# Optimization experiments

Hardware: AMD Instinct MI355X
Metric: run time of the kernel (lower is better)

The kernel has to match this reference:

```python
import jax, jax.numpy as jnp
import numpy as np

D = 768          # TGLU_hidden_dim == input_hidden_dim
E = 8            # num_experts
TOP_K = 2        # top_experts
N_ENT = 32       # num_entity
B = 16           # batch (mentions)
L = 128          # max_seq_len
EPS = 1e-5


def setup_inputs() -> dict:
    key = jax.random.key(0)
    ks = jax.random.split(key, 16)
    s = 0.02
    return {
        "entity_text_cls": jax.random.normal(ks[0], (N_ENT, D), jnp.float32),
        "entity_text_tokens": jax.random.normal(ks[1], (N_ENT, L, D), jnp.float32),
        "mention_text_cls": jax.random.normal(ks[2], (B, D), jnp.float32),
        "mention_text_tokens": jax.random.normal(ks[3], (B, L, D), jnp.float32),
        # SwitchMoE params: gate + per-expert Linear(dim -> output_dim)
        "gate_w": jax.random.normal(ks[4], (D, E), jnp.float32) * s,
        "gate_b": jnp.zeros((E,), jnp.float32),
        "exp_w": jax.random.normal(ks[5], (E, D, D), jnp.float32) * s,
        "exp_b": jnp.zeros((E, D), jnp.float32),
        # attention projections
        "wq": jax.random.normal(ks[6], (D, D), jnp.float32) * s,
        "bq": jnp.zeros((D,), jnp.float32),
        "wk": jax.random.normal(ks[7], (D, D), jnp.float32) * s,
        "bk": jnp.zeros((D,), jnp.float32),
        "wv": jax.random.normal(ks[8], (D, D), jnp.float32) * s,
        "bv": jnp.zeros((D,), jnp.float32),
        # LayerNorm params
        "ln_w": jnp.ones((D,), jnp.float32),
        "ln_b": jnp.zeros((D,), jnp.float32),
    }


def _switch_moe(x, gate_w, gate_b, exp_w, exp_b):
    # x: [n, s, D] -> [n, s, D]; top-k router, renormalized combine.
    logits = jnp.einsum("nsd,de->nse", x, gate_w) + gate_b
    probs = jax.nn.softmax(logits, axis=-1)
    vals, idx = jax.lax.top_k(probs, TOP_K)              # [n,s,k]
    vals = vals / jnp.sum(vals, axis=-1, keepdims=True)
    # combine weights over all experts (zero for unselected) -> dense mask form
    w = jnp.sum(jax.nn.one_hot(idx, E, dtype=x.dtype) * vals[..., None], axis=-2)  # [n,s,E]
    eo = jnp.einsum("nsd,edo->nseo", x, exp_w) + exp_b   # [n,s,E,D]
    return jnp.einsum("nse,nseo->nso", w, eo)


def _layernorm(x, w, b):
    mu = jnp.mean(x, axis=-1, keepdims=True)
    var = jnp.mean(jnp.square(x - mu), axis=-1, keepdims=True)
    return (x - mu) * jax.lax.rsqrt(var + EPS) * w + b


def reference(entity_text_cls, entity_text_tokens, mention_text_cls, mention_text_tokens,
              gate_w, gate_b, exp_w, exp_b, wq, bq, wk, bk, wv, bv, ln_w, ln_b):
    # prepend CLS, route through shared MoE
    ent = jnp.concatenate([entity_text_cls[:, None, :], entity_text_tokens], axis=1)   # [N,L+1,D]
    ent_moe = _switch_moe(ent, gate_w, gate_b, exp_w, exp_b)
    ent_cls_moe = ent_moe[:, 0, :]          # [N,D]
    ent_tok = ent_moe[:, 1:, :]             # [N,L,D]

    men = jnp.concatenate([mention_text_cls[:, None, :], mention_text_tokens], axis=1)  # [B,L+1,D]
    men_moe = _switch_moe(men, gate_w, gate_b, exp_w, exp_b)
    men_tok = men_moe[:, 1:, :]             # [B,L,D]

    q = jnp.einsum("nld,do->nlo", ent_tok, wq) + bq    # [N,L,D]
    k = jnp.einsum("bmd,do->bmo", men_tok, wk) + bk    # [B,L,D]
    v = jnp.einsum("bmd,do->bmo", men_tok, wv) + bv    # [B,L,D]

    # all-pairs entity x mention cross attention: [N,B,L,L]
    scores = jnp.einsum("nld,bmd->nblm", q, k) / jnp.sqrt(jnp.asarray(D, q.dtype))
    probs = jax.nn.softmax(scores, axis=-1)
    context = jnp.einsum("nblm,bmd->nbld", probs, v)   # [N,B,L,D]
    context = jnp.mean(context, axis=-2)               # [N,B,D]
    context = _layernorm(context, ln_w, ln_b)

    g2l = jnp.sum(ent_cls_moe[:, None, :] * context, axis=-1)   # [N,B]
    g2l = g2l.T                                                  # [B,N]
    g2g = mention_text_cls @ entity_text_cls.T                   # [B,N]
    return (g2l + g2g) / 2
```

## Files before the change

kernel.cpp:

```cpp
#include <hip/hip_runtime.h>
#include <math.h>

#define D 768
#define NE 8
#define NTOK 6192
#define MEN_TOK0 4128

typedef __attribute__((ext_vector_type(8))) short short8;
typedef __attribute__((ext_vector_type(4))) short short4b;
typedef __attribute__((ext_vector_type(4))) float floatx4;

__device__ __forceinline__ short f2bf(float f) {
  union { float f; unsigned u; } x; x.f = f;
  unsigned r = x.u + 0x7fffu + ((x.u >> 16) & 1u);
  return (short)(r >> 16);
}
__device__ __forceinline__ float bf2f(short s) {
  union { unsigned u; float f; } x; x.u = ((unsigned)(unsigned short)s) << 16;
  return x.f;
}

__device__ __forceinline__ void gload16(const short* g, short8* lds_base) {
  __builtin_amdgcn_global_load_lds(
      (const __attribute__((address_space(1))) unsigned int*)g,
      (__attribute__((address_space(3))) unsigned int*)lds_base,
      16, 0, 0);
}

#define PIPE_BAR(NSTR)                                            \
  do {                                                            \
    asm volatile("s_waitcnt vmcnt(" NSTR ")" ::: "memory");       \
    __builtin_amdgcn_sched_barrier(0);                            \
    __builtin_amdgcn_s_barrier();                                 \
    __builtin_amdgcn_sched_barrier(0);                            \
  } while (0)

__device__ __forceinline__ const float* token_row(int t,
    const float* __restrict__ ecls, const float* __restrict__ etok,
    const float* __restrict__ mcls, const float* __restrict__ mtok) {
  if (t < MEN_TOK0) {
    int n = t / 129, s = t - n * 129;
    return (s == 0) ? (ecls + n * D) : (etok + (size_t)(n * 128 + s - 1) * D);
  } else {
    int tm = t - MEN_TOK0;
    int b = tm / 129, s = tm - b * 129;
    return (s == 0) ? (mcls + b * D) : (mtok + (size_t)(b * 128 + s - 1) * D);
  }
}

__global__ __launch_bounds__(256) void prep_kernel(
    const float* __restrict__ ecls, const float* __restrict__ etok,
    const float* __restrict__ mcls, const float* __restrict__ mtok,
    const float* __restrict__ gate_w, const float* __restrict__ gate_b,
    const float* __restrict__ exp_w, const float* __restrict__ wq,
    const float* __restrict__ wk, const float* __restrict__ wv,
    int* __restrict__ te1, int* __restrict__ te2,
    float* __restrict__ tw1, float* __restrict__ tw2,
    short* __restrict__ Xb, short* __restrict__ expwT, short* __restrict__ wT) {
  __shared__ float tbuf[64][65];
  int bid = blockIdx.x;
  int tid = threadIdx.x;
  if (bid < 1548) {
    int t = bid * 4 + (tid >> 6);
    int lane = tid & 63;
    const float* xr = token_row(t, ecls, etok, mcls, mtok);
    float acc[NE];
#pragma unroll
    for (int e = 0; e < NE; ++e) acc[e] = 0.f;
#pragma unroll
    for (int it = 0; it < 3; ++it) {
      int d0 = lane * 4 + it * 256;
      floatx4 x = *(const floatx4*)(xr + d0);
      short4b xb;
#pragma unroll
      for (int q = 0; q < 4; ++q) {
        xb[q] = f2bf(x[q]);
        float xv = x[q];
#pragma unroll
        for (int e = 0; e < NE; ++e) acc[e] += xv * gate_w[(d0 + q) * NE + e];
      }
      *(short4b*)(Xb + (size_t)t * D + d0) = xb;
    }
#pragma unroll
    for (int e = 0; e < NE; ++e) {
#pragma unroll
      for (int off = 32; off > 0; off >>= 1) acc[e] += __shfl_down(acc[e], off);
    }
    if (lane == 0) {
      float lg[NE];
#pragma unroll
      for (int e = 0; e < NE; ++e) lg[e] = acc[e] + gate_b[e];
      int e1 = 0;
#pragma unroll
      for (int e = 1; e < NE; ++e) if (lg[e] > lg[e1]) e1 = e;
      int e2 = (e1 == 0) ? 1 : 0;
#pragma unroll
      for (int e = 0; e < NE; ++e) {
        if (e != e1 && lg[e] > lg[e2]) e2 = e;
      }
      float w1 = 1.f / (1.f + __expf(lg[e2] - lg[e1]));
      te1[t] = e1; te2[t] = e2;
      tw1[t] = w1; tw2[t] = 1.f - w1;
    }
  } else {
    int zz = bid - 1548;
    int z = zz / 144, rem = zz % 144;
    int k0 = (rem / 12) * 64, o0 = (rem % 12) * 64;
    const float* src; short* dst;
    if (z < 8) { src = exp_w + (size_t)z * D * D; dst = expwT + (size_t)z * D * D; }
    else { src = (z == 8) ? wq : (z == 9) ? wk : wv; dst = wT + (size_t)(z - 8) * D * D; }
    int tx = tid & 63, ty = tid >> 6;
#pragma unroll
    for (int i = 0; i < 16; ++i) {
      int k = i * 4 + ty;
      tbuf[k][tx] = src[(size_t)(k0 + k) * D + o0 + tx];
    }
    __syncthreads();
#pragma unroll
    for (int i = 0; i < 16; ++i) {
      int o = i * 4 + ty;
      dst[(size_t)(o0 + o) * D + k0 + tx] = f2bf(tbuf[tx][o]);
    }
  }
}

__global__ __launch_bounds__(1024) void route_kernel(
    const int* __restrict__ te1, const int* __restrict__ te2,
    int* __restrict__ lst_tok, int* __restrict__ slot1, int* __restrict__ slot2,
    int* __restrict__ cnt, int* __restrict__ basee) {
  __shared__ int hist[NE];
  __shared__ int base_s[NE];
  int tid = threadIdx.x;
  if (tid < NE) hist[tid] = 0;
  __syncthreads();
  for (int t = tid; t < NTOK; t += 1024) {
    atomicAdd(&hist[te1[t]], 1);
    atomicAdd(&hist[te2[t]], 1);
  }
  __syncthreads();
  if (tid == 0) {
    int acc = 0;
    for (int e = 0; e < NE; ++e) {
      base_s[e] = acc;
      cnt[e] = hist[e];
      basee[e] = acc;
      acc += hist[e];
    }
  }
  __syncthreads();
  if (tid < NE) hist[tid] = 0;
  __syncthreads();
  for (int t = tid; t < NTOK; t += 1024) {
    int e1 = te1[t], e2 = te2[t];
    int r1 = atomicAdd(&hist[e1], 1);
    int r2 = atomicAdd(&hist[e2], 1);
    int s1 = base_s[e1] + r1;
    int s2 = base_s[e2] + r2;
    slot1[t] = s1; slot2[t] = s2;
    lst_tok[s1] = t; lst_tok[s2] = t;
  }
}

__global__ __launch_bounds__(512, 4) void moe_kernel(
    const short* __restrict__ Xb, const short* __restrict__ expwT,
    const int* __restrict__ cnt, const int* __restrict__ basee,
    const int* __restrict__ lst_tok, short* __restrict__ EO) {
  int id = blockIdx.x;
  int e = id & 7;
  int r = id >> 3;
  int ob = r % 6;
  int tb = r / 6;
  int count = cnt[e];
  int t0 = tb * 128;
  if (t0 >= count) return;
  int o0 = ob * 128;
  int gb = basee[e];

  __shared__ short8 As[1536];
  __shared__ short8 Bs[1536];
  __shared__ int stok[128];

  int tid = threadIdx.x;
  int l = tid & 63, w = tid >> 6;
  int wr = w >> 1, wc = w & 1;

  if (tid < 128) {
    int p = t0 + tid;
    stok[tid] = lst_tok[gb + (p < count ? p : 0)];
  }
  __syncthreads();

  const short* Bg = expwT + (size_t)e * D * D;
  int srow = tid >> 2, scc = tid & 3;
  int csrc = (scc ^ ((srow >> 1) & 3)) * 8;
  const short* srcA = Xb + (size_t)stok[srow] * D + csrc;
  const short* srcB = Bg + (size_t)(o0 + srow) * D + csrc;

  floatx4 acc[2][4];
#pragma unroll
  for (int ai = 0; ai < 2; ++ai)
#pragma unroll
    for (int bj = 0; bj < 4; ++bj) acc[ai][bj] = (floatx4){0.f, 0.f, 0.f, 0.f};

  gload16(srcA, &As[w << 6]);
  gload16(srcB, &Bs[w << 6]);
  gload16(srcA + 32, &As[512 + (w << 6)]);
  gload16(srcB + 32, &Bs[512 + (w << 6)]);

  for (int it = 0; it < 24; ++it) {
    if (it < 23) PIPE_BAR("2"); else PIPE_BAR("0");
    int cur = (it % 3) << 9;
    if (it < 22) {
      int nb = ((it + 2) % 3) << 9;
      int k0n = (it + 2) * 32;
      gload16(srcA + k0n, &As[nb + (w << 6)]);
      gload16(srcB + k0n, &Bs[nb + (w << 6)]);
    }
    int kc = l >> 4;
    short8 a[2], bb[4];
#pragma unroll
    for (int ai = 0; ai < 2; ++ai) {
      int ar = wr * 32 + ai * 16 + (l & 15);
      a[ai] = As[cur + (ar << 2) + (kc ^ ((ar >> 1) & 3))];
    }
#pragma unroll
    for (int bj = 0; bj < 4; ++bj) {
      int br = wc * 64 + bj * 16 + (l & 15);
      bb[bj] = Bs[cur + (br << 2) + (kc ^ ((br >> 1) & 3))];
    }
    __builtin_amdgcn_s_setprio(1);
#pragma unroll
    for (int ai = 0; ai < 2; ++ai)
#pragma unroll
      for (int bj = 0; bj < 4; ++bj)
        acc[ai][bj] = __builtin_amdgcn_mfma_f32_16x16x32_bf16(a[ai], bb[bj], acc[ai][bj], 0, 0, 0);
    __builtin_amdgcn_s_setprio(0);
  }

#pragma unroll
  for (int ai = 0; ai < 2; ++ai) {
#pragma unroll
    for (int rr = 0; rr < 4; ++rr) {
      int rowl = wr * 32 + ai * 16 + ((l >> 4) << 2) + rr;
      int p = t0 + rowl;
      if (p < count) {
        size_t off = (size_t)(gb + p) * D;
#pragma unroll
        for (int bj = 0; bj < 4; ++bj) {
          int col = o0 + wc * 64 + bj * 16 + (l & 15);
          EO[off + col] = f2bf(acc[ai][bj][rr]);
        }
      }
    }
  }
}

__global__ __launch_bounds__(256) void combine_kernel(
    const short* __restrict__ EO,
    const int* __restrict__ te1, const int* __restrict__ te2,
    const float* __restrict__ tw1, const float* __restrict__ tw2,
    const int* __restrict__ slot1, const int* __restrict__ slot2,
    const float* __restrict__ exp_b, short* __restrict__ MOEb) {
  int idx = blockIdx.x * 256 + threadIdx.x;
  int t = idx / 96, cg = idx - t * 96;
  int c0 = cg * 8;
  int e1 = te1[t], e2 = te2[t];
  float w1 = tw1[t], w2 = tw2[t];
  short8 a = *(const short8*)(EO + (size_t)slot1[t] * D + c0);
  short8 b = *(const short8*)(EO + (size_t)slot2[t] * D + c0);
  const float* b1 = exp_b + e1 * D + c0;
  const float* b2 = exp_b + e2 * D + c0;
  short8 o;
#pragma unroll
  for (int j = 0; j < 8; ++j)
    o[j] = f2bf(w1 * (bf2f(a[j]) + b1[j]) + w2 * (bf2f(b[j]) + b2[j]));
  *(short8*)(MOEb + (size_t)t * D + c0) = o;
}

__global__ __launch_bounds__(512, 4) void qkv_kernel(
    const short* __restrict__ MOEb, const short* __restrict__ wT,
    const float* __restrict__ bq, const float* __restrict__ bk,
    const float* __restrict__ bv,
    short* __restrict__ Qb, short* __restrict__ Kb, short* __restrict__ Vb) {
  int id = blockIdx.x;
  int z, r;
  if (id < 192)      { z = 0; r = id; }
  else if (id < 288) { z = 1; r = id - 192; }
  else               { z = 2; r = id - 288; }
  int tb = r / 6, ob = r % 6;
  int o0 = ob * 128;
  int base = (z == 0) ? 0 : MEN_TOK0;
  const short* W = wT + (size_t)z * D * D;
  const float* bias = (z == 0) ? bq : (z == 1) ? bk : bv;
  const short* Ag = MOEb + (size_t)(base + tb * 129 + 1) * D;

  __shared__ short8 As[1536];
  __shared__ short8 Bs[1536];

  int tid = threadIdx.x;
  int l = tid & 63, w = tid >> 6;
  int wr = w >> 1, wc = w & 1;

  int srow = tid >> 2, scc = tid & 3;
  int csrc = (scc ^ ((srow >> 1) & 3)) * 8;
  const short* srcA = Ag + (size_t)srow * D + csrc;
  const short* srcB = W + (size_t)(o0 + srow) * D + csrc;

  floatx4 acc[2][4];
#pragma unroll
  for (int ai = 0; ai < 2; ++ai)
#pragma unroll
    for (int bj = 0; bj < 4; ++bj) acc[ai][bj] = (floatx4){0.f, 0.f, 0.f, 0.f};

  gload16(srcA, &As[w << 6]);
  gload16(srcB, &Bs[w << 6]);
  gload16(srcA + 32, &As[512 + (w << 6)]);
  gload16(srcB + 32, &Bs[512 + (w << 6)]);

  for (int it = 0; it < 24; ++it) {
    if (it < 23) PIPE_BAR("2"); else PIPE_BAR("0");
    int cur = (it % 3) << 9;
    if (it < 22) {
      int nb = ((it + 2) % 3) << 9;
      int k0n = (it + 2) * 32;
      gload16(srcA + k0n, &As[nb + (w << 6)]);
      gload16(srcB + k0n, &Bs[nb + (w << 6)]);
    }
    int kc = l >> 4;
    short8 a[2], bb[4];
#pragma unroll
    for (int ai = 0; ai < 2; ++ai) {
      int ar = wr * 32 + ai * 16 + (l & 15);
      a[ai] = As[cur + (ar << 2) + (kc ^ ((ar >> 1) & 3))];
    }
#pragma unroll
    for (int bj = 0; bj < 4; ++bj) {
      int br = wc * 64 + bj * 16 + (l & 15);
      bb[bj] = Bs[cur + (br << 2) + (kc ^ ((br >> 1) & 3))];
    }
    __builtin_amdgcn_s_setprio(1);
#pragma unroll
    for (int ai = 0; ai < 2; ++ai)
#pragma unroll
      for (int bj = 0; bj < 4; ++bj)
        acc[ai][bj] = __builtin_amdgcn_mfma_f32_16x16x32_bf16(a[ai], bb[bj], acc[ai][bj], 0, 0, 0);
    __builtin_amdgcn_s_setprio(0);
  }

#pragma unroll
  for (int ai = 0; ai < 2; ++ai) {
#pragma unroll
    for (int rr = 0; rr < 4; ++rr) {
      int rowl = wr * 32 + ai * 16 + ((l >> 4) << 2) + rr;
      size_t rglob = (size_t)tb * 128 + rowl;
#pragma unroll
      for (int bj = 0; bj < 4; ++bj) {
        int col = o0 + wc * 64 + bj * 16 + (l & 15);
        float v = acc[ai][bj][rr] + bias[col];
        if (z == 0)      Qb[rglob * D + col] = f2bf(v);
        else if (z == 1) Kb[rglob * D + col] = f2bf(v);
        else             Vb[rglob * D + col] = f2bf(v);
      }
    }
  }
}

__device__ __forceinline__ float blockSum512(float v, volatile float* red, int tid) {
#pragma unroll
  for (int off = 32; off > 0; off >>= 1) v += __shfl_down(v, off);
  __syncthreads();
  if ((tid & 63) == 0) red[tid >> 6] = v;
  __syncthreads();
  float s = 0.f;
#pragma unroll
  for (int i = 0; i < 8; ++i) s += red[i];
  return s;
}

__global__ __launch_bounds__(512, 4) void attn_kernel(
    const short* __restrict__ Qb, const short* __restrict__ Kb,
    const short* __restrict__ Vb, const short* __restrict__ MOEb,
    const float* __restrict__ ecls, const float* __restrict__ mcls,
    const float* __restrict__ ln_w, const float* __restrict__ ln_b,
    float* __restrict__ out) {
  int id = blockIdx.x;
  int n = id & 31, b = id >> 5;
  __shared__ short8 Qs[1536];
  __shared__ short8 Ks[1536];
  __shared__ float pb[128];
  __shared__ float red[8];
  float* smm = (float*)Qs;
  float* sss = (float*)Qs + 256;
  int tid = threadIdx.x;
  int l = tid & 63, w = tid >> 6;
  int wr = w >> 1, wc = w & 1;
  if (tid < 128) pb[tid] = 0.f;
  __syncthreads();

  floatx4 acc[2][4];
#pragma unroll
  for (int ai = 0; ai < 2; ++ai)
#pragma unroll
    for (int bj = 0; bj < 4; ++bj) acc[ai][bj] = (floatx4){0.f, 0.f, 0.f, 0.f};

  const short* qg = Qb + (size_t)n * 128 * D;
  const short* kg = Kb + (size_t)b * 128 * D;

  int srow = tid >> 2, scc = tid & 3;
  int csrc = (scc ^ ((srow >> 1) & 3)) * 8;
  const short* srcQ = qg + (size_t)srow * D + csrc;
  const short* srcK = kg + (size_t)srow * D + csrc;

  gload16(srcQ, &Qs[w << 6]);
  gload16(srcK, &Ks[w << 6]);
  gload16(srcQ + 32, &Qs[512 + (w << 6)]);
  gload16(srcK + 32, &Ks[512 + (w << 6)]);

  for (int it = 0; it < 24; ++it) {
    if (it < 23) PIPE_BAR("2"); else PIPE_BAR("0");
    int cur = (it % 3) << 9;
    if (it < 22) {
      int nb = ((it + 2) % 3) << 9;
      int k0n = (it + 2) * 32;
      gload16(srcQ + k0n, &Qs[nb + (w << 6)]);
      gload16(srcK + k0n, &Ks[nb + (w << 6)]);
    }
    int kc = l >> 4;
    short8 a[2], bb[4];
#pragma unroll
    for (int ai = 0; ai < 2; ++ai) {
      int ar = wr * 32 + ai * 16 + (l & 15);
      a[ai] = Qs[cur + (ar << 2) + (kc ^ ((ar >> 1) & 3))];
    }
#pragma unroll
    for (int bj = 0; bj < 4; ++bj) {
      int br = wc * 64 + bj * 16 + (l & 15);
      bb[bj] = Ks[cur + (br << 2) + (kc ^ ((br >> 1) & 3))];
    }
    __builtin_amdgcn_s_setprio(1);
#pragma unroll
    for (int ai = 0; ai < 2; ++ai)
#pragma unroll
      for (int bj = 0; bj < 4; ++bj)
        acc[ai][bj] = __builtin_amdgcn_mfma_f32_16x16x32_bf16(a[ai], bb[bj], acc[ai][bj], 0, 0, 0);
    __builtin_amdgcn_s_setprio(0);
  }

  const float scale = 0.03608439182435161f;
  float mloc[2][4], sloc[2][4];
#pragma unroll
  for (int ai = 0; ai < 2; ++ai) {
#pragma unroll
    for (int r = 0; r < 4; ++r) {
      float mx = -3.0e38f;
#pragma unroll
      for (int bj = 0; bj < 4; ++bj) mx = fmaxf(mx, acc[ai][bj][r]);
      mx = fmaxf(mx, __shfl_xor(mx, 1));
      mx = fmaxf(mx, __shfl_xor(mx, 2));
      mx = fmaxf(mx, __shfl_xor(mx, 4));
      mx = fmaxf(mx, __shfl_xor(mx, 8));
      float sm = 0.f;
#pragma unroll
      for (int bj = 0; bj < 4; ++bj) {
        float pv = __expf((acc[ai][bj][r] - mx) * scale);
        acc[ai][bj][r] = pv;
        sm += pv;
      }
      sm += __shfl_xor(sm, 1);
      sm += __shfl_xor(sm, 2);
      sm += __shfl_xor(sm, 4);
      sm += __shfl_xor(sm, 8);
      mloc[ai][r] = mx;
      sloc[ai][r] = sm;
    }
  }
  __syncthreads();
  if ((l & 15) == 0) {
#pragma unroll
    for (int ai = 0; ai < 2; ++ai)
#pragma unroll
      for (int r = 0; r < 4; ++r) {
        int row = wr * 32 + ai * 16 + ((l >> 4) << 2) + r;
        smm[row * 2 + wc] = mloc[ai][r];
        sss[row * 2 + wc] = sloc[ai][r];
      }
  }
  __syncthreads();

  float colsum[4];
#pragma unroll
  for (int bj = 0; bj < 4; ++bj) colsum[bj] = 0.f;
#pragma unroll
  for (int ai = 0; ai < 2; ++ai) {
#pragma unroll
    for (int r = 0; r < 4; ++r) {
      int row = wr * 32 + ai * 16 + ((l >> 4) << 2) + r;
      float m0 = smm[row * 2], m1 = smm[row * 2 + 1];
      float s0 = sss[row * 2], s1 = sss[row * 2 + 1];
      float M = fmaxf(m0, m1);
      float Z = s0 * __expf((m0 - M) * scale) + s1 * __expf((m1 - M) * scale);
      float fac = __expf((mloc[ai][r] - M) * scale) / Z;
#pragma unroll
      for (int bj = 0; bj < 4; ++bj) colsum[bj] += acc[ai][bj][r] * fac;
    }
  }
#pragma unroll
  for (int bj = 0; bj < 4; ++bj) {
    colsum[bj] += __shfl_xor(colsum[bj], 16);
    colsum[bj] += __shfl_xor(colsum[bj], 32);
  }
  if (l < 16) {
#pragma unroll
    for (int bj = 0; bj < 4; ++bj)
      atomicAdd(&pb[wc * 64 + bj * 16 + l], colsum[bj]);
  }
  __syncthreads();

  float ctx[4] = {0.f, 0.f, 0.f, 0.f};
  bool act = tid < 192;
  int d0 = tid << 2;
  if (act) {
    const short* vb = Vb + (size_t)b * 128 * D + d0;
    for (int m = 0; m < 128; ++m) {
      float p = pb[m];
      short4b v = *(const short4b*)(vb + (size_t)m * D);
#pragma unroll
      for (int j = 0; j < 4; ++j) ctx[j] += p * bf2f(v[j]);
    }
#pragma unroll
    for (int j = 0; j < 4; ++j) ctx[j] *= (1.f / 128.f);
  }

  float mu = blockSum512(ctx[0] + ctx[1] + ctx[2] + ctx[3], red, tid) * (1.f / 768.f);
  float c[4];
#pragma unroll
  for (int j = 0; j < 4; ++j) c[j] = ctx[j] - mu;
  float vs = act ? (c[0]*c[0] + c[1]*c[1] + c[2]*c[2] + c[3]*c[3]) : 0.f;
  float var = blockSum512(vs, red, tid) * (1.f / 768.f);
  float rstd = rsqrtf(var + 1e-5f);

  float g2l_p = 0.f, g2g_p = 0.f;
  if (act) {
    floatx4 lw = *(const floatx4*)(ln_w + d0);
    floatx4 lb = *(const floatx4*)(ln_b + d0);
    short4b em = *(const short4b*)(MOEb + (size_t)(n * 129) * D + d0);
    floatx4 mc = *(const floatx4*)(mcls + (size_t)b * D + d0);
    floatx4 ec = *(const floatx4*)(ecls + (size_t)n * D + d0);
#pragma unroll
    for (int j = 0; j < 4; ++j) {
      float cl = c[j] * rstd * lw[j] + lb[j];
      g2l_p += bf2f(em[j]) * cl;
      g2g_p += mc[j] * ec[j];
    }
  }
  float g2l = blockSum512(g2l_p, red, tid);
  float g2g = blockSum512(g2g_p, red, tid);
  if (tid == 0) out[b * 32 + n] = 0.5f * (g2l + g2g);
}

extern "C" void kernel_launch(void* const* d_in, const int* in_sizes, int n_in,
                              void* d_out, int out_size, void* d_ws, size_t ws_size,
                              hipStream_t stream) {
  const float* ecls   = (const float*)d_in[0];
  const float* etok   = (const float*)d_in[1];
  const float* mcls   = (const float*)d_in[2];
  const float* mtok   = (const float*)d_in[3];
  const float* gate_w = (const float*)d_in[4];
  const float* gate_b = (const float*)d_in[5];
  const float* exp_w  = (const float*)d_in[6];
  const float* exp_b  = (const float*)d_in[7];
  const float* wq     = (const float*)d_in[8];
  const float* bq     = (const float*)d_in[9];
  const float* wk     = (const float*)d_in[10];
  const float* bk     = (const float*)d_in[11];
  const float* wv     = (const float*)d_in[12];
  const float* bv     = (const float*)d_in[13];
  const float* ln_w   = (const float*)d_in[14];
  const float* ln_b   = (const float*)d_in[15];
  float* outp = (float*)d_out;

  char* ws = (char*)d_ws;
  short* Qb    = (short*)(ws + 0);
  short* Kb    = (short*)(ws + 6291456);
  short* Vb    = (short*)(ws + 9437184);
  short* Xb    = (short*)(ws + 12582912);
  short* EO    = (short*)(ws + 22093824);
  short* MOEb  = (short*)(ws + 41115648);
  short* expwT = (short*)(ws + 50626560);
  short* wT    = (short*)(ws + 60063744);
  int*   te1   = (int*)  (ws + 63602688);
  int*   te2   = (int*)  (ws + 63627456);
  float* tw1   = (float*)(ws + 63652224);
  float* tw2   = (float*)(ws + 63676992);
  int*   slot1 = (int*)  (ws + 63701760);
  int*   slot2 = (int*)  (ws + 63726528);
  int*   lst_tok = (int*)(ws + 63751296);
  int*   cnt   = (int*)  (ws + 63800832);
  int*   basee = (int*)  (ws + 63800864);

  prep_kernel<<<1548 + 1584, 256, 0, stream>>>(ecls, etok, mcls, mtok, gate_w, gate_b,
                                               exp_w, wq, wk, wv,
                                               te1, te2, tw1, tw2, Xb, expwT, wT);
  route_kernel<<<1, 1024, 0, stream>>>(te1, te2, lst_tok, slot1, slot2, cnt, basee);
  moe_kernel<<<49 * 6 * 8, 512, 0, stream>>>(Xb, expwT, cnt, basee, lst_tok, EO);
  combine_kernel<<<2322, 256, 0, stream>>>(EO, te1, te2, tw1, tw2, slot1, slot2,
                                           exp_b, MOEb);
  qkv_kernel<<<384, 512, 0, stream>>>(MOEb, wT, bq, bk, bv, Qb, Kb, Vb);
  attn_kernel<<<512, 512, 0, stream>>>(Qb, Kb, Vb, MOEb, ecls, mcls, ln_w, ln_b, outp);
}
```

Baseline: 121.6 us.

## Fuse MoE combine into expert GEMM epilogue and QKV operand load

Removes the separate combine kernel. The MoE GEMM epilogue now applies the expert bias and routing weight and writes to one of two per-slot buffers (R1/R2) indexed by token. The QKV GEMM loads both buffers, sums them in registers and stores the result to LDS, replacing the async global-to-LDS A loads with a two-stage double buffer synchronised by __syncthreads. The route kernel uses per-wave histograms and packs the slot bit into the list entry. This saves one launch and a full read/write pass over the combined activations, at the cost of a less pipelined QKV A-path and an extra bf16 rounding before the sum.

```diff
diff --git a/kernel.cpp b/kernel.cpp
--- a/kernel.cpp
+++ b/kernel.cpp
@@ -126,45 +126,50 @@
 
 __global__ __launch_bounds__(1024) void route_kernel(
     const int* __restrict__ te1, const int* __restrict__ te2,
-    int* __restrict__ lst_tok, int* __restrict__ slot1, int* __restrict__ slot2,
-    int* __restrict__ cnt, int* __restrict__ basee) {
-  __shared__ int hist[NE];
-  __shared__ int base_s[NE];
+    int* __restrict__ lst, int* __restrict__ cnt, int* __restrict__ basee) {
+  __shared__ int wh[16][8];
+  __shared__ int wbase[16][8];
+  __shared__ int ctr[16][8];
+  __shared__ int gbase[8];
+  __shared__ int etot[8];
   int tid = threadIdx.x;
-  if (tid < NE) hist[tid] = 0;
+  int w = tid >> 6;
+  if (tid < 128) { ((int*)wh)[tid] = 0; ((int*)ctr)[tid] = 0; }
   __syncthreads();
   for (int t = tid; t < NTOK; t += 1024) {
-    atomicAdd(&hist[te1[t]], 1);
-    atomicAdd(&hist[te2[t]], 1);
+    atomicAdd(&wh[w][te1[t]], 1);
+    atomicAdd(&wh[w][te2[t]], 1);
+  }
+  __syncthreads();
+  if (tid < NE) {
+    int e = tid, acc = 0;
+    for (int ww = 0; ww < 16; ++ww) { wbase[ww][e] = acc; acc += wh[ww][e]; }
+    etot[e] = acc;
+    cnt[e] = acc;
   }
   __syncthreads();
   if (tid == 0) {
     int acc = 0;
-    for (int e = 0; e < NE; ++e) {
-      base_s[e] = acc;
-      cnt[e] = hist[e];
-      basee[e] = acc;
-      acc += hist[e];
-    }
-  }
-  __syncthreads();
-  if (tid < NE) hist[tid] = 0;
+    for (int e = 0; e < NE; ++e) { gbase[e] = acc; basee[e] = acc; acc += etot[e]; }
+  }
   __syncthreads();
   for (int t = tid; t < NTOK; t += 1024) {
-    int e1 = te1[t], e2 = te2[t];
-    int r1 = atomicAdd(&hist[e1], 1);
-    int r2 = atomicAdd(&hist[e2], 1);
-    int s1 = base_s[e1] + r1;
-    int s2 = base_s[e2] + r2;
-    slot1[t] = s1; slot2[t] = s2;
-    lst_tok[s1] = t; lst_tok[s2] = t;
+    int e1 = te1[t];
+    int r1 = atomicAdd(&ctr[w][e1], 1);
+    lst[gbase[e1] + wbase[w][e1] + r1] = (t << 1);
+    int e2 = te2[t];
+    int r2 = atomicAdd(&ctr[w][e2], 1);
+    lst[gbase[e2] + wbase[w][e2] + r2] = (t << 1) | 1;
   }
 }
 
 __global__ __launch_bounds__(512, 4) void moe_kernel(
     const short* __restrict__ Xb, const short* __restrict__ expwT,
     const int* __restrict__ cnt, const int* __restrict__ basee,
-    const int* __restrict__ lst_tok, short* __restrict__ EO) {
+    const int* __restrict__ lst,
+    const float* __restrict__ tw1, const float* __restrict__ tw2,
+    const float* __restrict__ exp_b,
+    short* __restrict__ R1, short* __restrict__ R2) {
   int id = blockIdx.x;
   int e = id & 7;
   int r = id >> 3;
@@ -186,14 +191,14 @@
 
   if (tid < 128) {
     int p = t0 + tid;
-    stok[tid] = lst_tok[gb + (p < count ? p : 0)];
+    stok[tid] = lst[gb + (p < count ? p : 0)];
   }
   __syncthreads();
 
   const short* Bg = expwT + (size_t)e * D * D;
   int srow = tid >> 2, scc = tid & 3;
   int csrc = (scc ^ ((srow >> 1) & 3)) * 8;
-  const short* srcA = Xb + (size_t)stok[srow] * D + csrc;
+  const short* srcA = Xb + (size_t)(stok[srow] >> 1) * D + csrc;
   const short* srcB = Bg + (size_t)(o0 + srow) * D + csrc;
 
   floatx4 acc[2][4];
@@ -237,6 +242,7 @@
     __builtin_amdgcn_s_setprio(0);
   }
 
+  const float* be = exp_b + e * D;
 #pragma unroll
   for (int ai = 0; ai < 2; ++ai) {
 #pragma unroll
@@ -244,41 +250,24 @@
       int rowl = wr * 32 + ai * 16 + ((l >> 4) << 2) + rr;
       int p = t0 + rowl;
       if (p < count) {
-        size_t off = (size_t)(gb + p) * D;
+        int ent = stok[rowl];
+        int tok = ent >> 1;
+        float wt = (ent & 1) ? tw2[tok] : tw1[tok];
+        short* OUT = (ent & 1) ? R2 : R1;
+        size_t off = (size_t)tok * D;
 #pragma unroll
         for (int bj = 0; bj < 4; ++bj) {
           int col = o0 + wc * 64 + bj * 16 + (l & 15);
-          EO[off + col] = f2bf(acc[ai][bj][rr]);
+          OUT[off + col] = f2bf(wt * (acc[ai][bj][rr] + be[col]));
         }
       }
     }
   }
 }
 
-__global__ __launch_bounds__(256) void combine_kernel(
-    const short* __restrict__ EO,
-    const int* __restrict__ te1, const int* __restrict__ te2,
-    const float* __restrict__ tw1, const float* __restrict__ tw2,
-    const int* __restrict__ slot1, const int* __restrict__ slot2,
-    const float* __restrict__ exp_b, short* __restrict__ MOEb) {
-  int idx = blockIdx.x * 256 + threadIdx.x;
-  int t = idx / 96, cg = idx - t * 96;
-  int c0 = cg * 8;
-  int e1 = te1[t], e2 = te2[t];
-  float w1 = tw1[t], w2 = tw2[t];
-  short8 a = *(const short8*)(EO + (size_t)slot1[t] * D + c0);
-  short8 b = *(const short8*)(EO + (size_t)slot2[t] * D + c0);
-  const float* b1 = exp_b + e1 * D + c0;
-  const float* b2 = exp_b + e2 * D + c0;
-  short8 o;
-#pragma unroll
-  for (int j = 0; j < 8; ++j)
-    o[j] = f2bf(w1 * (bf2f(a[j]) + b1[j]) + w2 * (bf2f(b[j]) + b2[j]));
-  *(short8*)(MOEb + (size_t)t * D + c0) = o;
-}
-
 __global__ __launch_bounds__(512, 4) void qkv_kernel(
-    const short* __restrict__ MOEb, const short* __restrict__ wT,
+    const short* __restrict__ R1, const short* __restrict__ R2,
+    const short* __restrict__ wT,
     const float* __restrict__ bq, const float* __restrict__ bk,
     const float* __restrict__ bv,
     short* __restrict__ Qb, short* __restrict__ Kb, short* __restrict__ Vb) {
@@ -292,10 +281,10 @@
   int base = (z == 0) ? 0 : MEN_TOK0;
   const short* W = wT + (size_t)z * D * D;
   const float* bias = (z == 0) ? bq : (z == 1) ? bk : bv;
-  const short* Ag = MOEb + (size_t)(base + tb * 129 + 1) * D;
-
-  __shared__ short8 As[1536];
-  __shared__ short8 Bs[1536];
+  int tok0 = base + tb * 129 + 1;
+
+  __shared__ short8 As[1024];
+  __shared__ short8 Bs[1024];
 
   int tid = threadIdx.x;
   int l = tid & 63, w = tid >> 6;
@@ -303,7 +292,8 @@
 
   int srow = tid >> 2, scc = tid & 3;
   int csrc = (scc ^ ((srow >> 1) & 3)) * 8;
-  const short* srcA = Ag + (size_t)srow * D + csrc;
+  const short* pR1 = R1 + (size_t)(tok0 + srow) * D + csrc;
+  const short* pR2 = R2 + (size_t)(tok0 + srow) * D + csrc;
   const short* srcB = W + (size_t)(o0 + srow) * D + csrc;
 
   floatx4 acc[2][4];
@@ -312,39 +302,48 @@
 #pragma unroll
     for (int bj = 0; bj < 4; ++bj) acc[ai][bj] = (floatx4){0.f, 0.f, 0.f, 0.f};
 
-  gload16(srcA, &As[w << 6]);
   gload16(srcB, &Bs[w << 6]);
-  gload16(srcA + 32, &As[512 + (w << 6)]);
-  gload16(srcB + 32, &Bs[512 + (w << 6)]);
+  {
+    short8 a1 = *(const short8*)(pR1);
+    short8 a2 = *(const short8*)(pR2);
+    short8 v;
+#pragma unroll
+    for (int j = 0; j < 8; ++j) v[j] = f2bf(bf2f(a1[j]) + bf2f(a2[j]));
+    As[tid] = v;
+  }
+  __syncthreads();
 
   for (int it = 0; it < 24; ++it) {
-    if (it < 23) PIPE_BAR("2"); else PIPE_BAR("0");
-    int cur = (it % 3) << 9;
-    if (it < 22) {
-      int nb = ((it + 2) % 3) << 9;
-      int k0n = (it + 2) * 32;
-      gload16(srcA + k0n, &As[nb + (w << 6)]);
-      gload16(srcB + k0n, &Bs[nb + (w << 6)]);
-    }
+    int cur = it & 1;
+    if (it < 23) {
+      int k0n = (it + 1) * 32;
+      gload16(srcB + k0n, &Bs[((cur ^ 1) << 9) + (w << 6)]);
+      short8 a1 = *(const short8*)(pR1 + k0n);
+      short8 a2 = *(const short8*)(pR2 + k0n);
+      short8 v;
+#pragma unroll
+      for (int j = 0; j < 8; ++j) v[j] = f2bf(bf2f(a1[j]) + bf2f(a2[j]));
+      As[((cur ^ 1) << 9) + tid] = v;
+    }
+    int curA = cur << 9;
     int kc = l >> 4;
     short8 a[2], bb[4];
 #pragma unroll
     for (int ai = 0; ai < 2; ++ai) {
       int ar = wr * 32 + ai * 16 + (l & 15);
-      a[ai] = As[cur + (ar << 2) + (kc ^ ((ar >> 1) & 3))];
+      a[ai] = As[curA + (ar << 2) + (kc ^ ((ar >> 1) & 3))];
     }
 #pragma unroll
     for (int bj = 0; bj < 4; ++bj) {
       int br = wc * 64 + bj * 16 + (l & 15);
-      bb[bj] = Bs[cur + (br << 2) + (kc ^ ((br >> 1) & 3))];
-    }
-    __builtin_amdgcn_s_setprio(1);
+      bb[bj] = Bs[curA + (br << 2) + (kc ^ ((br >> 1) & 3))];
+    }
 #pragma unroll
     for (int ai = 0; ai < 2; ++ai)
 #pragma unroll
       for (int bj = 0; bj < 4; ++bj)
         acc[ai][bj] = __builtin_amdgcn_mfma_f32_16x16x32_bf16(a[ai], bb[bj], acc[ai][bj], 0, 0, 0);
-    __builtin_amdgcn_s_setprio(0);
+    __syncthreads();
   }
 
 #pragma unroll
@@ -379,7 +378,8 @@
 
 __global__ __launch_bounds__(512, 4) void attn_kernel(
     const short* __restrict__ Qb, const short* __restrict__ Kb,
-    const short* __restrict__ Vb, const short* __restrict__ MOEb,
+    const short* __restrict__ Vb,
+    const short* __restrict__ R1, const short* __restrict__ R2,
     const float* __restrict__ ecls, const float* __restrict__ mcls,
     const float* __restrict__ ln_w, const float* __restrict__ ln_b,
     float* __restrict__ out) {
@@ -543,13 +543,14 @@
   if (act) {
     floatx4 lw = *(const floatx4*)(ln_w + d0);
     floatx4 lb = *(const floatx4*)(ln_b + d0);
-    short4b em = *(const short4b*)(MOEb + (size_t)(n * 129) * D + d0);
+    short4b e1v = *(const short4b*)(R1 + (size_t)(n * 129) * D + d0);
+    short4b e2v = *(const short4b*)(R2 + (size_t)(n * 129) * D + d0);
     floatx4 mc = *(const floatx4*)(mcls + (size_t)b * D + d0);
     floatx4 ec = *(const floatx4*)(ecls + (size_t)n * D + d0);
 #pragma unroll
     for (int j = 0; j < 4; ++j) {
       float cl = c[j] * rstd * lw[j] + lb[j];
-      g2l_p += bf2f(em[j]) * cl;
+      g2l_p += (bf2f(e1v[j]) + bf2f(e2v[j])) * cl;
       g2g_p += mc[j] * ec[j];
     }
   }
@@ -584,27 +585,24 @@
   short* Kb    = (short*)(ws + 6291456);
   short* Vb    = (short*)(ws + 9437184);
   short* Xb    = (short*)(ws + 12582912);
-  short* EO    = (short*)(ws + 22093824);
-  short* MOEb  = (short*)(ws + 41115648);
-  short* expwT = (short*)(ws + 50626560);
-  short* wT    = (short*)(ws + 60063744);
-  int*   te1   = (int*)  (ws + 63602688);
-  int*   te2   = (int*)  (ws + 63627456);
-  float* tw1   = (float*)(ws + 63652224);
-  float* tw2   = (float*)(ws + 63676992);
-  int*   slot1 = (int*)  (ws + 63701760);
-  int*   slot2 = (int*)  (ws + 63726528);
-  int*   lst_tok = (int*)(ws + 63751296);
-  int*   cnt   = (int*)  (ws + 63800832);
-  int*   basee = (int*)  (ws + 63800864);
+  short* R1    = (short*)(ws + 22093824);
+  short* R2    = (short*)(ws + 31604736);
+  short* expwT = (short*)(ws + 41115648);
+  short* wT    = (short*)(ws + 50552832);
+  int*   te1   = (int*)  (ws + 54091776);
+  int*   te2   = (int*)  (ws + 54116544);
+  float* tw1   = (float*)(ws + 54141312);
+  float* tw2   = (float*)(ws + 54166080);
+  int*   lst   = (int*)  (ws + 54190848);
+  int*   cnt   = (int*)  (ws + 54240384);
+  int*   basee = (int*)  (ws + 54240416);
 
   prep_kernel<<<1548 + 1584, 256, 0, stream>>>(ecls, etok, mcls, mtok, gate_w, gate_b,
                                                exp_w, wq, wk, wv,
                                                te1, te2, tw1, tw2, Xb, expwT, wT);
-  route_kernel<<<1, 1024, 0, stream>>>(te1, te2, lst_tok, slot1, slot2, cnt, basee);
-  moe_kernel<<<49 * 6 * 8, 512, 0, stream>>>(Xb, expwT, cnt, basee, lst_tok, EO);
-  combine_kernel<<<2322, 256, 0, stream>>>(EO, te1, te2, tw1, tw2, slot1, slot2,
-                                           exp_b, MOEb);
-  qkv_kernel<<<384, 512, 0, stream>>>(MOEb, wT, bq, bk, bv, Qb, Kb, Vb);
-  attn_kernel<<<512, 512, 0, stream>>>(Qb, Kb, Vb, MOEb, ecls, mcls, ln_w, ln_b, outp);
-}
+  route_kernel<<<1, 1024, 0, stream>>>(te1, te2, lst, cnt, basee);
+  moe_kernel<<<49 * 6 * 8, 512, 0, stream>>>(Xb, expwT, cnt, basee, lst,
+                                             tw1, tw2, exp_b, R1, R2);
+  qkv_kernel<<<384, 512, 0, stream>>>(R1, R2, wT, bq, bk, bv, Qb, Kb, Vb);
+  attn_kernel<<<512, 512, 0, stream>>>(Qb, Kb, Vb, R1, R2, ecls, mcls, ln_w, ln_b, outp);
+}
```

Result: slower. 128.1 us (+5.4%).
